# Kernel tuning notes

Measured on AMD Instinct MI355X. Metric: run time of the kernel, lower is better.

Reference implementation:

```python
import jax, jax.numpy as jnp
import numpy as np

B, T, N, C = 64, 8192, 16, 2
ONSET_PROB = 0.005  # sparse onsets, realistic for piano rolls


def setup_inputs() -> dict:
    key = jax.random.key(0)
    k1, k2 = jax.random.split(key)
    vals = jax.random.uniform(k1, (B, T, N, C), dtype=jnp.float32)
    mask = jax.random.uniform(k2, (B, T, N, 1)) < ONSET_PROB
    onsets = jnp.where(mask, vals, 0.0)  # mostly-zero onset roll
    return {"onsets": onsets}


def reference(onsets):
    # onsets: (b, t, n, c). onset flag per frame: any note's channel-0 > 0.
    b, t, n, c = onsets.shape
    onset = jnp.max(onsets[..., 0], axis=-1) > 0  # (b, t) bool
    # Recurrence state = (state + 1) * (1 - onset) counts frames since the
    # last onset (0 at an onset frame), with a virtual onset at index -1.
    # Closed form: out[i] = i - (index of most recent onset <= i, else -1).
    ar = jnp.arange(t, dtype=jnp.int32)  # (t,)
    idx = jnp.where(onset, ar[None, :], -1)  # (b, t)
    last = jax.lax.cummax(idx, axis=1)  # (b, t) last onset index so far
    out = (ar[None, :] - last).astype(onsets.dtype)[..., None]  # (b, t, 1)
    return out
```

## Files before the change

kernel.cpp:

```cpp
#include <hip/hip_runtime.h>

#define B_ 64
#define T_ 8192
#define N_ 16
#define C_ 2
#define TILE 256
#define NT (T_ / TILE)

__global__ __launch_bounds__(TILE) void k1_scan(const float* __restrict__ onsets,
                                                float* __restrict__ out,
                                                int* __restrict__ tileMax,
                                                int* __restrict__ firstOnset) {
    const int blk  = blockIdx.x;
    const int b    = blk >> 5;
    const int tile = blk & (NT - 1);
    const int tid  = threadIdx.x;
    const int wave = tid >> 6;
    const int lane = tid & 63;

    __shared__ unsigned char flags[TILE];
    __shared__ int wmax[4];
    __shared__ int wfirst[4];

    const float4* base4 = (const float4*)onsets + ((size_t)(b * T_ + tile * TILE) << 3);

#pragma unroll
    for (int j = 0; j < 8; ++j) {
        float4 v = base4[(wave << 9) + (j << 6) + lane];
        float mm = fmaxf(v.x, v.z);
        mm = fmaxf(mm, __shfl_xor(mm, 1));
        mm = fmaxf(mm, __shfl_xor(mm, 2));
        mm = fmaxf(mm, __shfl_xor(mm, 4));
        if ((lane & 7) == 0)
            flags[(wave << 6) + (j << 3) + (lane >> 3)] = (mm > 0.0f) ? 1 : 0;
    }
    __syncthreads();

    const int t  = tile * TILE + tid;
    const bool on = flags[tid] != 0;
    int idx = on ? t : -1;
#pragma unroll
    for (int off = 1; off < 64; off <<= 1) {
        int u = __shfl_up(idx, off);
        if (lane >= off) idx = (u > idx) ? u : idx;
    }
    if (lane == 63) wmax[wave] = idx;
    unsigned long long bal = __ballot(on);
    if (lane == 0)
        wfirst[wave] = bal ? (tile * TILE + (wave << 6) + __ffsll(bal) - 1) : 0x7fffffff;
    __syncthreads();

    int carry = -1;
#pragma unroll
    for (int w = 0; w < 4; ++w) {
        int v = wmax[w];
        if (w < wave && v > carry) carry = v;
    }
    const int last = (carry > idx) ? carry : idx;
    out[b * T_ + t] = (float)(t - last);

    if (tid == 0) {
        int bm = wmax[0], f = wfirst[0];
#pragma unroll
        for (int w = 1; w < 4; ++w) {
            bm = (wmax[w] > bm) ? wmax[w] : bm;
            f  = (wfirst[w] < f) ? wfirst[w] : f;
        }
        tileMax[blk]    = bm;
        firstOnset[blk] = f;
    }
}

__global__ __launch_bounds__(TILE) void k2_fixup(const int* __restrict__ tileMax,
                                                 const int* __restrict__ firstOnset,
                                                 float* __restrict__ out) {
    const int blk  = blockIdx.x;
    const int b    = blk >> 5;
    const int tile = blk & (NT - 1);
    const int tid  = threadIdx.x;

    __shared__ int carry_s;
    if (tid < 64) {
        int v = (tid < tile) ? tileMax[(b << 5) + tid] : -1;
#pragma unroll
        for (int off = 32; off; off >>= 1) {
            int u = __shfl_xor(v, off);
            v = (u > v) ? u : v;
        }
        if (tid == 0) carry_s = v;
    }
    __syncthreads();

    const int f = firstOnset[blk];
    const int t = tile * TILE + tid;
    if (t < f) out[b * T_ + t] = (float)(t - carry_s);
}

extern "C" void kernel_launch(void* const* d_in, const int* in_sizes, int n_in,
                              void* d_out, int out_size, void* d_ws, size_t ws_size,
                              hipStream_t stream) {
    const float* onsets = (const float*)d_in[0];
    float* out = (float*)d_out;

    int* tileMax    = (int*)d_ws;
    int* firstOnset = tileMax + B_ * NT;

    dim3 grid(B_ * NT);
    k1_scan<<<grid, TILE, 0, stream>>>(onsets, out, tileMax, firstOnset);
    k2_fixup<<<grid, TILE, 0, stream>>>(tileMax, firstOnset, out);
}
```

Before: 93.63 us.

## Fuse scan and fixup kernels using per-tile backward lookback for carry

Replaces the two-kernel scheme (per-tile scan, then a fixup pass using tile maxima) with one kernel. A tile whose first frame is not an onset scans the input backwards in 32-frame chunks until it finds the most recent onset, and uses that as its carry. This removes the second launch, the workspace round-trip and the partial rewrite of the output. In exchange, tiles re-read some input, and very sparse inputs could force long serial lookbacks.

```diff
diff --git a/kernel.cpp b/kernel.cpp
--- a/kernel.cpp
+++ b/kernel.cpp
@@ -3,14 +3,11 @@
 #define B_ 64
 #define T_ 8192
 #define N_ 16
-#define C_ 2
 #define TILE 256
 #define NT (T_ / TILE)
 
-__global__ __launch_bounds__(TILE) void k1_scan(const float* __restrict__ onsets,
-                                                float* __restrict__ out,
-                                                int* __restrict__ tileMax,
-                                                int* __restrict__ firstOnset) {
+__global__ __launch_bounds__(TILE) void k_fused(const float* __restrict__ onsets,
+                                                float* __restrict__ out) {
     const int blk  = blockIdx.x;
     const int b    = blk >> 5;
     const int tile = blk & (NT - 1);
@@ -20,9 +17,10 @@
 
     __shared__ unsigned char flags[TILE];
     __shared__ int wmax[4];
-    __shared__ int wfirst[4];
+    __shared__ int wtmp[4];
 
-    const float4* base4 = (const float4*)onsets + ((size_t)(b * T_ + tile * TILE) << 3);
+    const float4* row4  = (const float4*)onsets + (size_t)b * (T_ * 8);
+    const float4* base4 = row4 + (size_t)(tile * TILE) * 8;
 
 #pragma unroll
     for (int j = 0; j < 8; ++j) {
@@ -45,9 +43,7 @@
         if (lane >= off) idx = (u > idx) ? u : idx;
     }
     if (lane == 63) wmax[wave] = idx;
-    unsigned long long bal = __ballot(on);
-    if (lane == 0)
-        wfirst[wave] = bal ? (tile * TILE + (wave << 6) + __ffsll(bal) - 1) : 0x7fffffff;
+    const bool needCarry = (tile > 0) && (flags[0] == 0);
     __syncthreads();
 
     int carry = -1;
@@ -56,44 +52,40 @@
         int v = wmax[w];
         if (w < wave && v > carry) carry = v;
     }
+
+    if (needCarry) {
+        int cs = tile * TILE - 32;
+        for (;;) {
+            float4 v = row4[(size_t)cs * 8 + tid];
+            float mm = fmaxf(v.x, v.z);
+            mm = fmaxf(mm, __shfl_xor(mm, 1));
+            mm = fmaxf(mm, __shfl_xor(mm, 2));
+            mm = fmaxf(mm, __shfl_xor(mm, 4));
+            unsigned long long bal = __ballot(((lane & 7) == 0) && (mm > 0.0f));
+            if (lane == 0) {
+                int wbest = -1;
+                if (bal) {
+                    int hb = 63 - __clzll(bal);
+                    wbest = cs + (wave << 3) + (hb >> 3);
+                }
+                wtmp[wave] = wbest;
+            }
+            __syncthreads();
+            int bbest = wtmp[0];
+            bbest = (wtmp[1] > bbest) ? wtmp[1] : bbest;
+            bbest = (wtmp[2] > bbest) ? wtmp[2] : bbest;
+            bbest = (wtmp[3] > bbest) ? wtmp[3] : bbest;
+            if (bbest >= 0 || cs == 0) {
+                if (bbest > carry) carry = bbest;
+                break;
+            }
+            cs -= 32;
+            __syncthreads();
+        }
+    }
+
     const int last = (carry > idx) ? carry : idx;
     out[b * T_ + t] = (float)(t - last);
-
-    if (tid == 0) {
-        int bm = wmax[0], f = wfirst[0];
-#pragma unroll
-        for (int w = 1; w < 4; ++w) {
-            bm = (wmax[w] > bm) ? wmax[w] : bm;
-            f  = (wfirst[w] < f) ? wfirst[w] : f;
-        }
-        tileMax[blk]    = bm;
-        firstOnset[blk] = f;
-    }
-}
-
-__global__ __launch_bounds__(TILE) void k2_fixup(const int* __restrict__ tileMax,
-                                                 const int* __restrict__ firstOnset,
-                                                 float* __restrict__ out) {
-    const int blk  = blockIdx.x;
-    const int b    = blk >> 5;
-    const int tile = blk & (NT - 1);
-    const int tid  = threadIdx.x;
-
-    __shared__ int carry_s;
-    if (tid < 64) {
-        int v = (tid < tile) ? tileMax[(b << 5) + tid] : -1;
-#pragma unroll
-        for (int off = 32; off; off >>= 1) {
-            int u = __shfl_xor(v, off);
-            v = (u > v) ? u : v;
-        }
-        if (tid == 0) carry_s = v;
-    }
-    __syncthreads();
-
-    const int f = firstOnset[blk];
-    const int t = tile * TILE + tid;
-    if (t < f) out[b * T_ + t] = (float)(t - carry_s);
 }
 
 extern "C" void kernel_launch(void* const* d_in, const int* in_sizes, int n_in,
@@ -101,11 +93,5 @@
                               hipStream_t stream) {
     const float* onsets = (const float*)d_in[0];
     float* out = (float*)d_out;
-
-    int* tileMax    = (int*)d_ws;
-    int* firstOnset = tileMax + B_ * NT;
-
-    dim3 grid(B_ * NT);
-    k1_scan<<<grid, TILE, 0, stream>>>(onsets, out, tileMax, firstOnset);
-    k2_fixup<<<grid, TILE, 0, stream>>>(tileMax, firstOnset, out);
+    k_fused<<<dim3(B_ * NT), TILE, 0, stream>>>(onsets, out);
 }
```

After: 91.66 us. -2.1%, faster.
